# Performance work log

Hardware: AMD Instinct MI355X
Metric: run time of the kernel (lower is better)

Reference implementation:

```python
import jax, jax.numpy as jnp
import numpy as np

EPS = 1e-5

def _layer_norm(x, g, b):
    mu = jnp.mean(x, axis=-1, keepdims=True)
    var = jnp.mean(jnp.square(x - mu), axis=-1, keepdims=True)
    return (x - mu) * jax.lax.rsqrt(var + EPS) * g + b

def setup_inputs() -> dict:
    key = jax.random.key(0)
    Bsz, N, H = 2, 384, 128
    ks = jax.random.split(key, 16)
    s = 1.0 / np.sqrt(H)
    d = {
        'h_nodes': jax.random.normal(ks[0], (Bsz, N, H), jnp.float32),
        'h_edges': jax.random.normal(ks[1], (Bsz, N, N, H), jnp.float32),
        'adj_matrix_mask': (jax.random.uniform(ks[2], (Bsz, N, N)) < 0.5).astype(jnp.float32),
    }
    for i, nm in enumerate(['U', 'V', 'A', 'B', 'C']):
        d[nm + '_w'] = jax.random.normal(ks[3 + 2 * i], (H, H), jnp.float32) * s
        d[nm + '_b'] = jax.random.normal(ks[4 + 2 * i], (H,), jnp.float32) * s
    d['gh'] = jnp.ones((H,), jnp.float32); d['bh'] = jnp.zeros((H,), jnp.float32)
    d['ge'] = jnp.ones((H,), jnp.float32); d['be'] = jnp.zeros((H,), jnp.float32)
    return d

def reference(h_nodes, h_edges, adj_matrix_mask, U_w, U_b, V_w, V_b, A_w, A_b, B_w, B_b, C_w, C_b, gh, bh, ge, be):
    # torch Linear: y = x @ W^T + b
    Uh = h_nodes @ U_w.T + U_b            # [B,N,H]
    Vh = h_nodes @ V_w.T + V_b            # [B,N,H] (j features)
    Ah = h_nodes @ A_w.T + A_b
    Bh = h_nodes @ B_w.T + B_b
    Ce = h_edges @ C_w.T + C_b            # [B,N,N,H]
    e_upd = Ah[:, :, None, :] + Bh[:, None, :, :] + Ce   # [B,N,N,H]
    gates = jax.nn.sigmoid(e_upd)
    msgs = gates * Vh[:, None, :, :] * adj_matrix_mask[..., None]
    agg = jnp.sum(msgs, axis=2)           # sum over j -> [B,N,H]
    h_upd = jax.nn.relu(_layer_norm(Uh + agg, gh, bh))
    e_act = jax.nn.relu(_layer_norm(e_upd, ge, be))
    return (h_nodes + h_upd, h_edges + e_act)
```

## Files before the change

kernel.cpp:

```cpp
#include <hip/hip_runtime.h>
#include <hip/hip_bf16.h>

typedef __bf16 bf16_t;
typedef __bf16 bf16x8 __attribute__((ext_vector_type(8)));
typedef __bf16 bf16x4 __attribute__((ext_vector_type(4)));
typedef float f32x4 __attribute__((ext_vector_type(4)));

#define HD 128
#define NN 384
#define ROWS 768
#define SZ 98304
#define JC 3

__device__ inline int detect_f32(const void* p) {
    const unsigned short* u = (const unsigned short*)p;
    int bad = 0;
    #pragma unroll
    for (int k = 0; k < 128; ++k) {
        int e = (u[k] >> 7) & 0xFF;
        bad += (e < 110 || e > 135) ? 1 : 0;
    }
    return bad >= 16 ? 1 : 0;
}

__global__ __launch_bounds__(64) void detect_kernel(const void* p, float* ws) {
    if (threadIdx.x == 0)
        *(int*)((char*)ws + (size_t)7 * SZ * 4) = detect_f32(p);
}

__device__ inline int read_flag(const float* ws) {
    return *(const int*)((const char*)ws + (size_t)7 * SZ * 4);
}

template<int CTRL>
__device__ __attribute__((always_inline)) inline float dpp_add(float x) {
    int xi = __builtin_bit_cast(int, x);
    int yi = __builtin_amdgcn_update_dpp(0, xi, CTRL, 0xF, 0xF, true);
    return x + __builtin_bit_cast(float, yi);
}
__device__ __attribute__((always_inline)) inline float row16_sum(float x) {
    x = dpp_add<0xB1>(x);
    x = dpp_add<0x4E>(x);
    x = dpp_add<0x124>(x);
    x = dpp_add<0x128>(x);
    return x;
}

__device__ __attribute__((always_inline)) inline void ld8(const float* p, float* o) {
    f32x4 a = *(const f32x4*)p;
    f32x4 b = *(const f32x4*)(p + 4);
    o[0] = a[0]; o[1] = a[1]; o[2] = a[2]; o[3] = a[3];
    o[4] = b[0]; o[5] = b[1]; o[6] = b[2]; o[7] = b[3];
}
__device__ __attribute__((always_inline)) inline void ld8(const bf16_t* p, float* o) {
    bf16x8 v = *(const bf16x8*)p;
    #pragma unroll
    for (int e = 0; e < 8; ++e) o[e] = (float)v[e];
}
__device__ __attribute__((always_inline)) inline bf16x8 ld8b(const float* p) {
    f32x4 a = *(const f32x4*)p;
    f32x4 b = *(const f32x4*)(p + 4);
    bf16x8 v;
    #pragma unroll
    for (int e = 0; e < 4; ++e) { v[e] = (bf16_t)a[e]; v[e + 4] = (bf16_t)b[e]; }
    return v;
}
__device__ __attribute__((always_inline)) inline bf16x8 ld8b(const bf16_t* p) { return *(const bf16x8*)p; }
__device__ __attribute__((always_inline)) inline bf16x4 ld4b(const float* p) {
    f32x4 a = *(const f32x4*)p;
    bf16x4 v;
    #pragma unroll
    for (int e = 0; e < 4; ++e) v[e] = (bf16_t)a[e];
    return v;
}
__device__ __attribute__((always_inline)) inline bf16x4 ld4b(const bf16_t* p) { return *(const bf16x4*)p; }

template<typename T>
__device__ void node_body(float* x,
    const T* h_nodes, const T* Uw, const T* Ub, const T* Vw, const T* Vb,
    const T* Aw, const T* Ab, const T* Bw, const T* Bb, const T* Cb,
    float* ws)
{
    const int row = blockIdx.x, m = blockIdx.y, t = threadIdx.x;
    x[t] = (float)h_nodes[row * HD + t];
    __syncthreads();

    const T* Ws[4] = {Aw, Bw, Vw, Uw};
    float bias;
    if (m == 0)      bias = (float)Ab[t] + (float)Cb[t];
    else if (m == 1) bias = (float)Bb[t];
    else if (m == 2) bias = (float)Vb[t];
    else             bias = (float)Ub[t];

    float acc = bias;
    const T* W = Ws[m] + (size_t)t * HD;
    #pragma unroll
    for (int kk = 0; kk < 16; ++kk) {
        float w8[8];
        ld8(W + kk * 8, w8);
        #pragma unroll
        for (int e = 0; e < 8; ++e) acc = fmaf(x[kk * 8 + e], w8[e], acc);
    }
    ws[m * SZ + row * HD + t] = acc;
}

__global__ __launch_bounds__(128) void node_linear(
    const void* h_nodes, const void* Uw, const void* Ub, const void* Vw, const void* Vb,
    const void* Aw, const void* Ab, const void* Bw, const void* Bb, const void* Cb,
    float* __restrict__ ws)
{
    __shared__ __align__(16) float x[HD];
    if (read_flag(ws))
        node_body<float>(x, (const float*)h_nodes, (const float*)Uw, (const float*)Ub,
                         (const float*)Vw, (const float*)Vb, (const float*)Aw, (const float*)Ab,
                         (const float*)Bw, (const float*)Bb, (const float*)Cb, ws);
    else
        node_body<bf16_t>(x, (const bf16_t*)h_nodes, (const bf16_t*)Uw, (const bf16_t*)Ub,
                          (const bf16_t*)Vw, (const bf16_t*)Vb, (const bf16_t*)Aw, (const bf16_t*)Ab,
                          (const bf16_t*)Bw, (const bf16_t*)Bb, (const bf16_t*)Cb, ws);
}

struct Smem {
    bf16_t sCw[128 * 128];
    float sAhC[HD], sGe[HD], sBe[HD];
    float sAgg[8][HD];
};

template<typename T>
__device__ void edge_body(Smem& sm,
    const T* __restrict__ h_edges, const T* __restrict__ adj,
    const T* __restrict__ Cw, const T* __restrict__ ge, const T* __restrict__ be,
    const float* __restrict__ ws, float* __restrict__ wagg, float* __restrict__ out)
{
    const int i = blockIdx.x, jc = blockIdx.y, b = blockIdx.z;
    const int bi = b * NN + i;
    const int t = threadIdx.x;
    const int l = t & 63, w = t >> 6;
    const int lr = l & 15, lg = l >> 4;
    const int hbase = lg * 4;

    {
        const int slot = t & 15;
        #pragma unroll
        for (int p = 0; p < 4; ++p) {
            const int row = p * 32 + (t >> 4);
            bf16x8 v = ld8b(&Cw[(size_t)row * HD + slot * 8]);
            *(bf16x8*)((char*)sm.sCw + row * 256 + ((slot ^ (row & 15)) << 4)) = v;
        }
    }
    if (t < HD) {
        sm.sAhC[t] = ws[0 * SZ + bi * HD + t];
        sm.sGe[t]  = (float)ge[t];
        sm.sBe[t]  = (float)be[t];
    }

    __syncthreads();

    const T* Ebase = h_edges + (size_t)bi * NN * HD;
    const int j = jc * 128 + w * 16 + lr;
    const T* Erow = &Ebase[(size_t)j * HD];

    const float mk = (float)adj[(size_t)bi * NN + j];
    bf16x4 res[8];
    #pragma unroll
    for (int ct = 0; ct < 8; ++ct)
        res[ct] = ld4b(&Erow[ct * 16 + hbase]);

    const float* Bhrow = ws + 1 * SZ + ((size_t)b * NN + j) * HD;
    const float* Vhrow = ws + 2 * SZ + ((size_t)b * NN + j) * HD;
    f32x4 bhv[8], vhv[8];
    #pragma unroll
    for (int ct = 0; ct < 8; ++ct) {
        bhv[ct] = *(const f32x4*)&Bhrow[ct * 16 + hbase];
        vhv[ct] = *(const f32x4*)&Vhrow[ct * 16 + hbase];
    }

    f32x4 acc[8];
    #pragma unroll
    for (int ct = 0; ct < 8; ++ct) acc[ct] = (f32x4){0.f, 0.f, 0.f, 0.f};
    #pragma unroll
    for (int ks = 0; ks < 4; ++ks) {
        bf16x8 a = ld8b(&Erow[ks * 32 + lg * 8]);
        #pragma unroll
        for (int ct = 0; ct < 8; ++ct) {
            bf16x8 Bf = *(const bf16x8*)((const char*)sm.sCw +
                          (ct * 16 + lr) * 256 + ((((ks << 2) | lg) ^ lr) << 4));
            acc[ct] = __builtin_amdgcn_mfma_f32_16x16x32_bf16(Bf, a, acc[ct], 0, 0, 0);
        }
    }

    float* Orow = out + SZ + ((size_t)bi * NN + j) * HD;

    float sum = 0.f, ssq = 0.f;
    #pragma unroll
    for (int ct = 0; ct < 8; ++ct) {
        f32x4 e = acc[ct];
        f32x4 av = *(const f32x4*)&sm.sAhC[ct * 16 + hbase];
        e = e + av + bhv[ct];
        acc[ct] = e;
        #pragma unroll
        for (int r = 0; r < 4; ++r) { sum += e[r]; ssq = fmaf(e[r], e[r], ssq); }
    }
    sum += __shfl_xor(sum, 16); ssq += __shfl_xor(ssq, 16);
    sum += __shfl_xor(sum, 32); ssq += __shfl_xor(ssq, 32);
    const float mean = sum * (1.f / HD);
    const float rstd = rsqrtf(ssq * (1.f / HD) - mean * mean + 1e-5f);

    f32x4 agg4[8];
    #pragma unroll
    for (int ct = 0; ct < 8; ++ct) {
        f32x4 ge4 = *(const f32x4*)&sm.sGe[ct * 16 + hbase];
        f32x4 be4 = *(const f32x4*)&sm.sBe[ct * 16 + hbase];
        f32x4 o;
        #pragma unroll
        for (int r = 0; r < 4; ++r) {
            const float ee = acc[ct][r];
            const float g = 1.f / (1.f + exp2f(ee * -1.44269504f));
            agg4[ct][r] = g * mk * vhv[ct][r];
            float a = (ee - mean) * rstd;
            a = fmaf(a, ge4[r], be4[r]);
            a = fmaxf(a, 0.f);
            o[r] = (float)res[ct][r] + a;
        }
        *(f32x4*)&Orow[ct * 16 + hbase] = o;
    }

    #pragma unroll
    for (int ct = 0; ct < 8; ++ct)
        #pragma unroll
        for (int r = 0; r < 4; ++r)
            agg4[ct][r] = row16_sum(agg4[ct][r]);
    if (lr == 0) {
        #pragma unroll
        for (int ct = 0; ct < 8; ++ct)
            *(f32x4*)&sm.sAgg[w][ct * 16 + hbase] = agg4[ct];
    }
    __syncthreads();

    if (t < HD) {
        float p = sm.sAgg[0][t] + sm.sAgg[1][t] + sm.sAgg[2][t] + sm.sAgg[3][t]
                + sm.sAgg[4][t] + sm.sAgg[5][t] + sm.sAgg[6][t] + sm.sAgg[7][t];
        wagg[((size_t)jc * ROWS + bi) * HD + t] = p;
    }
}

__global__ __launch_bounds__(512) void edge_kernel(
    const void* h_edges, const void* adj, const void* Cw,
    const void* ge, const void* be,
    float* __restrict__ ws, float* __restrict__ out)
{
    __shared__ Smem sm;
    float* wagg = ws + 4 * SZ;
    if (read_flag(ws))
        edge_body<float>(sm, (const float*)h_edges, (const float*)adj, (const float*)Cw,
                         (const float*)ge, (const float*)be, ws, wagg, out);
    else
        edge_body<bf16_t>(sm, (const bf16_t*)h_edges, (const bf16_t*)adj, (const bf16_t*)Cw,
                          (const bf16_t*)ge, (const bf16_t*)be, ws, wagg, out);
}

template<typename T>
__device__ void node_upd_body(const T* h_nodes, const T* gh, const T* bh,
                              const float* ws, float* out)
{
    const int bi = blockIdx.x, t = threadIdx.x;
    float x0 = ws[3 * SZ + bi * HD + t];
    float x1 = ws[3 * SZ + bi * HD + t + 64];
    #pragma unroll
    for (int jc = 0; jc < JC; ++jc) {
        const float* p = ws + 4 * SZ + ((size_t)jc * ROWS + bi) * HD;
        x0 += p[t];
        x1 += p[t + 64];
    }
    float sum = x0 + x1;
    float ssq = x0 * x0 + x1 * x1;
    #pragma unroll
    for (int off = 1; off < 64; off <<= 1) {
        sum += __shfl_xor(sum, off);
        ssq += __shfl_xor(ssq, off);
    }
    const float mean = sum * (1.f / HD);
    const float rstd = rsqrtf(ssq * (1.f / HD) - mean * mean + 1e-5f);
    float a0 = fmaf((x0 - mean) * rstd, (float)gh[t],      (float)bh[t]);
    float a1 = fmaf((x1 - mean) * rstd, (float)gh[t + 64], (float)bh[t + 64]);
    a0 = fmaxf(a0, 0.f);
    a1 = fmaxf(a1, 0.f);
    out[bi * HD + t]      = (float)h_nodes[bi * HD + t]      + a0;
    out[bi * HD + t + 64] = (float)h_nodes[bi * HD + t + 64] + a1;
}

__global__ __launch_bounds__(64) void node_update(
    const void* h_nodes, const void* gh, const void* bh,
    const float* __restrict__ ws, float* __restrict__ out)
{
    if (read_flag(ws))
        node_upd_body<float>((const float*)h_nodes, (const float*)gh, (const float*)bh, ws, out);
    else
        node_upd_body<bf16_t>((const bf16_t*)h_nodes, (const bf16_t*)gh, (const bf16_t*)bh, ws, out);
}

extern "C" void kernel_launch(void* const* d_in, const int* in_sizes, int n_in,
                              void* d_out, int out_size, void* d_ws, size_t ws_size,
                              hipStream_t stream)
{
    float* ws = (float*)d_ws;
    float* out = (float*)d_out;

    detect_kernel<<<dim3(1), dim3(64), 0, stream>>>(d_in[0], ws);
    node_linear<<<dim3(ROWS, 4), dim3(128), 0, stream>>>(
        d_in[0], d_in[3], d_in[4], d_in[5], d_in[6], d_in[7], d_in[8],
        d_in[9], d_in[10], d_in[12], ws);
    edge_kernel<<<dim3(NN, JC, 2), dim3(512), 0, stream>>>(
        d_in[1], d_in[2], d_in[11], d_in[15], d_in[16], ws, out);
    node_update<<<dim3(ROWS), dim3(64), 0, stream>>>(
        d_in[0], d_in[13], d_in[14], ws, out);
}
```

Baseline: 145.9 us.

## Store Bh/Vh as bf16, pad Cw LDS pitch, fast rcp sigmoid, raise occupancy

Result: faster. 139.8 us (-4.1%).

```diff
diff --git a/kernel.cpp b/kernel.cpp
--- a/kernel.cpp
+++ b/kernel.cpp
@@ -11,6 +11,7 @@
 #define ROWS 768
 #define SZ 98304
 #define JC 3
+#define CWPITCH 272
 
 __device__ inline int detect_f32(const void* p) {
     const unsigned short* u = (const unsigned short*)p;
@@ -101,7 +102,10 @@
         #pragma unroll
         for (int e = 0; e < 8; ++e) acc = fmaf(x[kk * 8 + e], w8[e], acc);
     }
-    ws[m * SZ + row * HD + t] = acc;
+    if (m == 1 || m == 2)
+        ((bf16_t*)(ws + (size_t)m * SZ))[row * HD + t] = (bf16_t)acc;
+    else
+        ws[(size_t)m * SZ + row * HD + t] = acc;
 }
 
 __global__ __launch_bounds__(128) void node_linear(
@@ -121,7 +125,7 @@
 }
 
 struct Smem {
-    bf16_t sCw[128 * 128];
+    bf16_t sCw[128 * (CWPITCH / 2)];
     float sAhC[HD], sGe[HD], sBe[HD];
     float sAgg[8][HD];
 };
@@ -145,7 +149,7 @@
         for (int p = 0; p < 4; ++p) {
             const int row = p * 32 + (t >> 4);
             bf16x8 v = ld8b(&Cw[(size_t)row * HD + slot * 8]);
-            *(bf16x8*)((char*)sm.sCw + row * 256 + ((slot ^ (row & 15)) << 4)) = v;
+            *(bf16x8*)((char*)sm.sCw + row * CWPITCH + slot * 16) = v;
         }
     }
     if (t < HD) {
@@ -166,13 +170,13 @@
     for (int ct = 0; ct < 8; ++ct)
         res[ct] = ld4b(&Erow[ct * 16 + hbase]);
 
-    const float* Bhrow = ws + 1 * SZ + ((size_t)b * NN + j) * HD;
-    const float* Vhrow = ws + 2 * SZ + ((size_t)b * NN + j) * HD;
-    f32x4 bhv[8], vhv[8];
+    const bf16_t* Bhrow = (const bf16_t*)(ws + 1 * SZ) + ((size_t)b * NN + j) * HD;
+    const bf16_t* Vhrow = (const bf16_t*)(ws + 2 * SZ) + ((size_t)b * NN + j) * HD;
+    bf16x4 bhv[8], vhv[8];
     #pragma unroll
     for (int ct = 0; ct < 8; ++ct) {
-        bhv[ct] = *(const f32x4*)&Bhrow[ct * 16 + hbase];
-        vhv[ct] = *(const f32x4*)&Vhrow[ct * 16 + hbase];
+        bhv[ct] = *(const bf16x4*)&Bhrow[ct * 16 + hbase];
+        vhv[ct] = *(const bf16x4*)&Vhrow[ct * 16 + hbase];
     }
 
     f32x4 acc[8];
@@ -184,7 +188,7 @@
         #pragma unroll
         for (int ct = 0; ct < 8; ++ct) {
             bf16x8 Bf = *(const bf16x8*)((const char*)sm.sCw +
-                          (ct * 16 + lr) * 256 + ((((ks << 2) | lg) ^ lr) << 4));
+                          (ct * 16 + lr) * CWPITCH + (((ks << 2) | lg)) * 16);
             acc[ct] = __builtin_amdgcn_mfma_f32_16x16x32_bf16(Bf, a, acc[ct], 0, 0, 0);
         }
     }
@@ -196,7 +200,8 @@
     for (int ct = 0; ct < 8; ++ct) {
         f32x4 e = acc[ct];
         f32x4 av = *(const f32x4*)&sm.sAhC[ct * 16 + hbase];
-        e = e + av + bhv[ct];
+        #pragma unroll
+        for (int r = 0; r < 4; ++r) e[r] = e[r] + av[r] + (float)bhv[ct][r];
         acc[ct] = e;
         #pragma unroll
         for (int r = 0; r < 4; ++r) { sum += e[r]; ssq = fmaf(e[r], e[r], ssq); }
@@ -215,8 +220,8 @@
         #pragma unroll
         for (int r = 0; r < 4; ++r) {
             const float ee = acc[ct][r];
-            const float g = 1.f / (1.f + exp2f(ee * -1.44269504f));
-            agg4[ct][r] = g * mk * vhv[ct][r];
+            const float g = __builtin_amdgcn_rcpf(1.f + exp2f(ee * -1.44269504f));
+            agg4[ct][r] = g * mk * (float)vhv[ct][r];
             float a = (ee - mean) * rstd;
             a = fmaf(a, ge4[r], be4[r]);
             a = fmaxf(a, 0.f);
@@ -244,7 +249,7 @@
     }
 }
 
-__global__ __launch_bounds__(512) void edge_kernel(
+__global__ __launch_bounds__(512, 2) void edge_kernel(
     const void* h_edges, const void* adj, const void* Cw,
     const void* ge, const void* be,
     float* __restrict__ ws, float* __restrict__ out)
```
